# Kernel optimization log

Measured on AMD Instinct MI355X. Metric: run time of the kernel, lower is better.

## Reference

```python
import jax, jax.numpy as jnp
import numpy as np


def _temperature():
    # Reproduce the per-class temperature from RIDE.__init__
    cls_num_list = np.array([705, 717, 281, 4772, 1982, 1290, 2524], dtype=np.float64)
    p = cls_num_list / cls_num_list.sum()
    C = len(cls_num_list)
    w = C * p * 0.015 + 1 - 0.015
    w = w / w.max()
    return jnp.asarray(1.5 * w, dtype=jnp.float32)[None, :]  # (1, C)


def setup_inputs() -> dict:
    key = jax.random.key(0)
    k1, k2, k3, k4, k5 = jax.random.split(key, 5)
    N, C = 2097152, 7
    return {
        "outputs1": jax.random.normal(k1, (N, C), dtype=jnp.float32),
        "outputs2": jax.random.normal(k2, (N, C), dtype=jnp.float32),
        "outputs3": jax.random.normal(k3, (N, C), dtype=jnp.float32),
        "outputs4": jax.random.normal(k4, (N, C), dtype=jnp.float32),
        "targets": jax.random.randint(k5, (N,), 0, C, dtype=jnp.int64),
    }


def reference(outputs1, outputs2, outputs3, outputs4, targets):
    # targets is unused by the original loss math (only logits enter the KL terms).
    T = _temperature()                       # (1, C), broadcasts over batch
    mT2 = jnp.mean(T * T)                    # scalar: mean over classes of T^2

    z0 = outputs1 / T                        # (N, C)
    q = jax.nn.softmax(z0, axis=-1)          # teacher probs
    logq = jax.nn.log_softmax(z0, axis=-1)

    def kl_mean(out_j):
        # KLDivLoss(reduction='mean') over a single-sample (1, C) slice == mean over C
        lp = jax.nn.log_softmax(out_j / T, axis=-1)
        return jnp.mean(q * (logq - lp), axis=-1)  # (N,)

    cost = kl_mean(outputs2) + kl_mean(outputs3) + kl_mean(outputs4)  # (N,)
    # KD_loss (scalar) * T * T then .mean(1) == KD_loss * mean(T^2); d = cost/3
    loss = cost * mT2 / 3.0
    return jnp.mean(loss)
```

## Files before the change

### kernel.cpp

```cpp
#include <hip/hip_runtime.h>


struct RideConsts {
    float invT[7];
    float scale;
};

template <int CPW>
__global__ __launch_bounds__(256, 5) void ride_main(
    const float* __restrict__ x1, const float* __restrict__ x2,
    const float* __restrict__ x3, const float* __restrict__ x4,
    float* __restrict__ partials, RideConsts cst)
{
    __shared__ __align__(16) float lds[4][1792];

    const int t = threadIdx.x;
    const int w = t >> 6;
    const int L = t & 63;
    float* myLds = lds[w];

    const float* xs[4] = {x1, x2, x3, x4};
    const int waveId = blockIdx.x * 4 + w;

    const long long cbase = (long long)waveId * CPW * 448 + L;

    float4 v0, v1, v2, v3, v4, v5, v6;

    {
        const float4* gp = (const float4*)xs[0] + cbase;
        v0 = gp[0];   v1 = gp[64];  v2 = gp[128]; v3 = gp[192];
        v4 = gp[256]; v5 = gp[320]; v6 = gp[384];
    }

    float q[28], qlogq[4];
    float cost = 0.0f;

#pragma unroll
    for (int c = 0; c < CPW; ++c) {
#pragma unroll
        for (int a = 0; a < 4; ++a) {
            {
                float4* dst = (float4*)myLds;
                dst[0 * 64 + L] = v0; dst[1 * 64 + L] = v1;
                dst[2 * 64 + L] = v2; dst[3 * 64 + L] = v3;
                dst[4 * 64 + L] = v4; dst[5 * 64 + L] = v5;
                dst[6 * 64 + L] = v6;
            }
            __builtin_amdgcn_sched_barrier(0);

            if (c * 4 + a + 1 < CPW * 4) {
                const int na = (a + 1) & 3;
                const int nc = (a == 3) ? c + 1 : c;
                const float4* gp = (const float4*)xs[na] + (cbase + nc * 448);
                v0 = gp[0];   v1 = gp[64];  v2 = gp[128]; v3 = gp[192];
                v4 = gp[256]; v5 = gp[320]; v6 = gp[384];
            }
            __builtin_amdgcn_sched_barrier(0);

            if (a == 0) {
#pragma unroll
                for (int rr = 0; rr < 4; ++rr) {
                    const float* r = &myLds[7 * L + 448 * rr];
                    float z[7], m = -1e30f;
#pragma unroll
                    for (int cc = 0; cc < 7; ++cc) {
                        z[cc] = r[cc] * cst.invT[cc];
                        m = fmaxf(m, z[cc]);
                    }
                    float S = 0.0f;
#pragma unroll
                    for (int cc = 0; cc < 7; ++cc) {
                        float e = __expf(z[cc] - m);
                        q[7 * rr + cc] = e; S += e;
                    }
                    const float invS = 1.0f / S, logS = __logf(S);
                    float sq = 0.0f;
#pragma unroll
                    for (int cc = 0; cc < 7; ++cc) {
                        float qq = q[7 * rr + cc] * invS;
                        q[7 * rr + cc] = qq;
                        sq += qq * (z[cc] - m - logS);
                    }
                    qlogq[rr] = sq;
                }
            } else {
#pragma unroll
                for (int rr = 0; rr < 4; ++rr) {
                    const float* r = &myLds[7 * L + 448 * rr];
                    float z[7], m = -1e30f;
#pragma unroll
                    for (int cc = 0; cc < 7; ++cc) {
                        z[cc] = r[cc] * cst.invT[cc];
                        m = fmaxf(m, z[cc]);
                    }
                    float S = 0.0f, dot = 0.0f;
#pragma unroll
                    for (int cc = 0; cc < 7; ++cc) {
                        S   += __expf(z[cc] - m);
                        dot += q[7 * rr + cc] * z[cc];
                    }
                    cost += qlogq[rr] - dot + m + __logf(S);
                }
            }
        }
    }

    cost *= (1.0f / 7.0f);
    cost *= cst.scale;

#pragma unroll
    for (int off = 32; off > 0; off >>= 1)
        cost += __shfl_down(cost, off, 64);
    if (L == 0) partials[waveId] = cost;
}

__global__ __launch_bounds__(256) void ride_reduce(
    const float* __restrict__ p, float* __restrict__ out, int n4)
{
    const float4* p4 = (const float4*)p;
    float s = 0.0f;
    for (int i = threadIdx.x; i < n4; i += 256) {
        float4 v = p4[i];
        s += (v.x + v.y) + (v.z + v.w);
    }
#pragma unroll
    for (int off = 32; off > 0; off >>= 1)
        s += __shfl_down(s, off, 64);
    __shared__ float red[4];
    if ((threadIdx.x & 63) == 0) red[threadIdx.x >> 6] = s;
    __syncthreads();
    if (threadIdx.x == 0) out[0] = red[0] + red[1] + red[2] + red[3];
}

extern "C" void kernel_launch(void* const* d_in, const int* in_sizes, int n_in,
                              void* d_out, int out_size, void* d_ws, size_t ws_size,
                              hipStream_t stream)
{
    const float* x1 = (const float*)d_in[0];
    const float* x2 = (const float*)d_in[1];
    const float* x3 = (const float*)d_in[2];
    const float* x4 = (const float*)d_in[3];

    const int N = in_sizes[0] / 7;

    RideConsts cst;
    {
        const double cls[7] = {705, 717, 281, 4772, 1982, 1290, 2524};
        double sum = 0.0;
        for (int c = 0; c < 7; ++c) sum += cls[c];
        double w[7], wmax = 0.0;
        for (int c = 0; c < 7; ++c) {
            const double p = cls[c] / sum;
            w[c] = 7.0 * p * 0.015 + 1.0 - 0.015;
            if (w[c] > wmax) wmax = w[c];
        }
        double mT2 = 0.0;
        for (int c = 0; c < 7; ++c) {
            const float T = (float)(1.5 * (w[c] / wmax));
            cst.invT[c] = 1.0f / T;
            mT2 += (double)T * (double)T;
        }
        mT2 /= 7.0;
        cst.scale = (float)(mT2 / (3.0 * (double)N));
    }

    constexpr int CPW = 1;
    const int nWaves = (N / 256) / CPW;
    const int grid   = nWaves / 4;

    float* partials = (float*)d_ws;

    ride_main<CPW><<<grid, 256, 0, stream>>>(x1, x2, x3, x4, partials, cst);
    ride_reduce<<<1, 256, 0, stream>>>(partials, (float*)d_out, nWaves / 4);
}
```

Before: 224.4 us.

## Drop LDS staging, sum student logits, apply teacher probabilities once

Removes the per-wave LDS transpose and software-pipelined prefetch. Each lane now loads its 4 rows directly as 7 contiguous float4s and keeps them in registers. Algebraically, the three student passes accumulate the scaled logits and the max+logsumexp terms, and the teacher softmax is applied once at the end as a single dot product with the summed logits. The 1/7 factor is folded into the host scale. This trades coalesced strided loads for per-lane contiguous 112-byte loads that rely on cache line reuse. It removes LDS traffic, sched barriers and repeated q dot products, and lets more loads be in flight at once.

Result: slower. 235.2 us (+4.8%).

```diff
diff --git a/kernel.cpp b/kernel.cpp
--- a/kernel.cpp
+++ b/kernel.cpp
@@ -6,106 +6,88 @@
     float scale;
 };
 
-template <int CPW>
 __global__ __launch_bounds__(256, 5) void ride_main(
     const float* __restrict__ x1, const float* __restrict__ x2,
     const float* __restrict__ x3, const float* __restrict__ x4,
     float* __restrict__ partials, RideConsts cst)
 {
-    __shared__ __align__(16) float lds[4][1792];
-
     const int t = threadIdx.x;
     const int w = t >> 6;
     const int L = t & 63;
-    float* myLds = lds[w];
-
-    const float* xs[4] = {x1, x2, x3, x4};
     const int waveId = blockIdx.x * 4 + w;
 
-    const long long cbase = (long long)waveId * CPW * 448 + L;
+    const size_t base = (size_t)waveId * 448 + (size_t)L * 7;
 
-    float4 v0, v1, v2, v3, v4, v5, v6;
+    float zsum[28];
+#pragma unroll
+    for (int i = 0; i < 28; ++i) zsum[i] = 0.0f;
+    float mls[4] = {0.0f, 0.0f, 0.0f, 0.0f};
 
-    {
-        const float4* gp = (const float4*)xs[0] + cbase;
-        v0 = gp[0];   v1 = gp[64];  v2 = gp[128]; v3 = gp[192];
-        v4 = gp[256]; v5 = gp[320]; v6 = gp[384];
-    }
-
-    float q[28], qlogq[4];
-    float cost = 0.0f;
-
+    const float* xs[3] = {x2, x3, x4};
 #pragma unroll
-    for (int c = 0; c < CPW; ++c) {
+    for (int j = 0; j < 3; ++j) {
+        const float4* gp = (const float4*)xs[j] + base;
+        float fv[28];
 #pragma unroll
-        for (int a = 0; a < 4; ++a) {
-            {
-                float4* dst = (float4*)myLds;
-                dst[0 * 64 + L] = v0; dst[1 * 64 + L] = v1;
-                dst[2 * 64 + L] = v2; dst[3 * 64 + L] = v3;
-                dst[4 * 64 + L] = v4; dst[5 * 64 + L] = v5;
-                dst[6 * 64 + L] = v6;
+        for (int k = 0; k < 7; ++k) {
+            const float4 v = gp[k];
+            fv[4 * k + 0] = v.x; fv[4 * k + 1] = v.y;
+            fv[4 * k + 2] = v.z; fv[4 * k + 3] = v.w;
+        }
+#pragma unroll
+        for (int r = 0; r < 4; ++r) {
+            float z[7], m = -1e30f;
+#pragma unroll
+            for (int cc = 0; cc < 7; ++cc) {
+                z[cc] = fv[7 * r + cc] * cst.invT[cc];
+                m = fmaxf(m, z[cc]);
             }
-            __builtin_amdgcn_sched_barrier(0);
-
-            if (c * 4 + a + 1 < CPW * 4) {
-                const int na = (a + 1) & 3;
-                const int nc = (a == 3) ? c + 1 : c;
-                const float4* gp = (const float4*)xs[na] + (cbase + nc * 448);
-                v0 = gp[0];   v1 = gp[64];  v2 = gp[128]; v3 = gp[192];
-                v4 = gp[256]; v5 = gp[320]; v6 = gp[384];
+            float S = 0.0f;
+#pragma unroll
+            for (int cc = 0; cc < 7; ++cc) {
+                S += __expf(z[cc] - m);
+                zsum[7 * r + cc] += z[cc];
             }
-            __builtin_amdgcn_sched_barrier(0);
-
-            if (a == 0) {
-#pragma unroll
-                for (int rr = 0; rr < 4; ++rr) {
-                    const float* r = &myLds[7 * L + 448 * rr];
-                    float z[7], m = -1e30f;
-#pragma unroll
-                    for (int cc = 0; cc < 7; ++cc) {
-                        z[cc] = r[cc] * cst.invT[cc];
-                        m = fmaxf(m, z[cc]);
-                    }
-                    float S = 0.0f;
-#pragma unroll
-                    for (int cc = 0; cc < 7; ++cc) {
-                        float e = __expf(z[cc] - m);
-                        q[7 * rr + cc] = e; S += e;
-                    }
-                    const float invS = 1.0f / S, logS = __logf(S);
-                    float sq = 0.0f;
-#pragma unroll
-                    for (int cc = 0; cc < 7; ++cc) {
-                        float qq = q[7 * rr + cc] * invS;
-                        q[7 * rr + cc] = qq;
-                        sq += qq * (z[cc] - m - logS);
-                    }
-                    qlogq[rr] = sq;
-                }
-            } else {
-#pragma unroll
-                for (int rr = 0; rr < 4; ++rr) {
-                    const float* r = &myLds[7 * L + 448 * rr];
-                    float z[7], m = -1e30f;
-#pragma unroll
-                    for (int cc = 0; cc < 7; ++cc) {
-                        z[cc] = r[cc] * cst.invT[cc];
-                        m = fmaxf(m, z[cc]);
-                    }
-                    float S = 0.0f, dot = 0.0f;
-#pragma unroll
-                    for (int cc = 0; cc < 7; ++cc) {
-                        S   += __expf(z[cc] - m);
-                        dot += q[7 * rr + cc] * z[cc];
-                    }
-                    cost += qlogq[rr] - dot + m + __logf(S);
-                }
-            }
+            mls[r] += m + __logf(S);
         }
     }
 
-    cost *= (1.0f / 7.0f);
+    float cost = 0.0f;
+    {
+        const float4* gp = (const float4*)x1 + base;
+        float fv[28];
+#pragma unroll
+        for (int k = 0; k < 7; ++k) {
+            const float4 v = gp[k];
+            fv[4 * k + 0] = v.x; fv[4 * k + 1] = v.y;
+            fv[4 * k + 2] = v.z; fv[4 * k + 3] = v.w;
+        }
+#pragma unroll
+        for (int r = 0; r < 4; ++r) {
+            float z[7], m = -1e30f;
+#pragma unroll
+            for (int cc = 0; cc < 7; ++cc) {
+                z[cc] = fv[7 * r + cc] * cst.invT[cc];
+                m = fmaxf(m, z[cc]);
+            }
+            float e[7], S = 0.0f;
+#pragma unroll
+            for (int cc = 0; cc < 7; ++cc) {
+                e[cc] = __expf(z[cc] - m);
+                S += e[cc];
+            }
+            const float invS = 1.0f / S, logS = __logf(S);
+            float sq = 0.0f, dot = 0.0f;
+#pragma unroll
+            for (int cc = 0; cc < 7; ++cc) {
+                const float qq = e[cc] * invS;
+                sq  += qq * (z[cc] - m - logS);
+                dot += qq * zsum[7 * r + cc];
+            }
+            cost += 3.0f * sq - dot + mls[r];
+        }
+    }
+
     cost *= cst.scale;
 
 #pragma unroll
@@ -161,15 +143,14 @@
             mT2 += (double)T * (double)T;
         }
         mT2 /= 7.0;
-        cst.scale = (float)(mT2 / (3.0 * (double)N));
+        cst.scale = (float)(mT2 / (3.0 * (double)N * 7.0));
     }
 
-    constexpr int CPW = 1;
-    const int nWaves = (N / 256) / CPW;
+    const int nWaves = N / 256;
     const int grid   = nWaves / 4;
 
     float* partials = (float*)d_ws;
 
-    ride_main<CPW><<<grid, 256, 0, stream>>>(x1, x2, x3, x4, partials, cst);
+    ride_main<<<grid, 256, 0, stream>>>(x1, x2, x3, x4, partials, cst);
     ride_reduce<<<1, 256, 0, stream>>>(partials, (float*)d_out, nWaves / 4);
 }
```
